# Performance work log

Hardware: AMD Instinct MI355X
Metric: run time of the kernel (lower is better)

The kernel has to match this reference:

```python
import jax, jax.numpy as jnp
import numpy as np

B, S, H, NH = 2, 2048, 2048, 16
HD = H // NH  # head_dim = 128


def setup_inputs() -> dict:
    key = jax.random.key(0)
    ks = jax.random.split(key, 6)
    scale = 1.0 / np.sqrt(H)
    hidden_state = jax.random.normal(ks[0], (B, S, H), dtype=jnp.float32)
    # upper-triangular (strictly above diagonal) = 1 -> masked positions
    causal_mask = jnp.triu(jnp.ones((S, S), dtype=jnp.float32), k=1)[None, None]
    Wq = jax.random.normal(ks[1], (H, H), dtype=jnp.float32) * scale
    Wk = jax.random.normal(ks[2], (H, H), dtype=jnp.float32) * scale
    Wv = jax.random.normal(ks[3], (H, H), dtype=jnp.float32) * scale
    Wo = jax.random.normal(ks[4], (H, H), dtype=jnp.float32) * scale
    zeros = jnp.zeros((H,), dtype=jnp.float32)
    return {"hidden_state": hidden_state, "causal_mask": causal_mask,
            "Wq": Wq, "bq": zeros, "Wk": Wk, "bk": zeros,
            "Wv": Wv, "bv": zeros, "Wo": Wo, "bo": zeros}


def reference(hidden_state, causal_mask, Wq, bq, Wk, bk, Wv, bv, Wo, bo):
    b, s, h = hidden_state.shape
    q = (hidden_state @ Wq.T + bq).reshape(b, s, NH, HD).transpose(0, 2, 1, 3)  # [B,NH,S,HD]
    k = (hidden_state @ Wk.T + bk).reshape(b, s, NH, HD).transpose(0, 2, 1, 3)
    v = (hidden_state @ Wv.T + bv).reshape(b, s, NH, HD).transpose(0, 2, 1, 3)
    scores = jnp.einsum('bhqd,bhkd->bhqk', q, k) / jnp.sqrt(jnp.float32(HD))
    scores = scores + causal_mask * (-1e9)
    probs = jax.nn.softmax(scores, axis=-1)
    out = jnp.einsum('bhqk,bhkd->bhqd', probs, v)
    out = out.transpose(0, 2, 1, 3).reshape(b, s, h)
    return out @ Wo.T + bo
```

## Files before the change

kernel.cpp:

```cpp
#include <hip/hip_runtime.h>
#include <hip/hip_bf16.h>
#include <stdint.h>

#define B_   2
#define S_   2048
#define H_   2048
#define NH_  16
#define HD_  128
#define MTOT (B_*S_)

typedef __attribute__((ext_vector_type(8))) short bf16x8;
typedef __attribute__((ext_vector_type(4))) short bf16x4;
typedef __attribute__((ext_vector_type(4))) float f32x4;

__device__ __forceinline__ void gload_lds16(const void* g, void* l) {
    __builtin_amdgcn_global_load_lds(
        (const __attribute__((address_space(1))) void*)g,
        (__attribute__((address_space(3))) void*)l, 16, 0, 0);
}

__device__ __forceinline__ unsigned short f2bfu(float x) {
    __hip_bfloat16 h = __float2bfloat16(x);
    return *reinterpret_cast<unsigned short*>(&h);
}
__device__ __forceinline__ int packbf(float a, float b) {
    return (int)f2bfu(a) | ((int)f2bfu(b) << 16);
}

#define BAR()  asm volatile("s_barrier" ::: "memory")
#define WLG0() asm volatile("s_waitcnt lgkmcnt(0)" ::: "memory")
#define WVM(n) asm volatile("s_waitcnt vmcnt(" #n ")" ::: "memory")

__global__ void castk(const float* __restrict__ in, __hip_bfloat16* __restrict__ out, int n4) {
    int i = blockIdx.x * 256 + threadIdx.x;
    if (i < n4) {
        float4 v = *(const float4*)(in + (size_t)i * 4);
        out[(size_t)i*4 + 0] = __float2bfloat16(v.x);
        out[(size_t)i*4 + 1] = __float2bfloat16(v.y);
        out[(size_t)i*4 + 2] = __float2bfloat16(v.z);
        out[(size_t)i*4 + 3] = __float2bfloat16(v.w);
    }
}

__global__ void castw4(const float* __restrict__ w0, const float* __restrict__ w1,
                       const float* __restrict__ w2, const float* __restrict__ w3,
                       __hip_bfloat16* o0, __hip_bfloat16* o1,
                       __hip_bfloat16* o2, __hip_bfloat16* o3, int n4) {
    const float* in; __hip_bfloat16* out;
    switch (blockIdx.y) {
        case 0:  in = w0; out = o0; break;
        case 1:  in = w1; out = o1; break;
        case 2:  in = w2; out = o2; break;
        default: in = w3; out = o3; break;
    }
    int i = blockIdx.x * 256 + threadIdx.x;
    if (i < n4) {
        float4 v = *(const float4*)(in + (size_t)i * 4);
        out[(size_t)i*4 + 0] = __float2bfloat16(v.x);
        out[(size_t)i*4 + 1] = __float2bfloat16(v.y);
        out[(size_t)i*4 + 2] = __float2bfloat16(v.z);
        out[(size_t)i*4 + 3] = __float2bfloat16(v.w);
    }
}

template<int SMEMB, int BF16OUT>
__device__ __forceinline__ void gemm_body(const __hip_bfloat16* __restrict__ Ablk,
                                          const __hip_bfloat16* __restrict__ Wblk,
                                          const float* __restrict__ bias,
                                          void* __restrict__ Cout,
                                          int N, int K, int br, int bc, bool vt)
{
    __shared__ __align__(16) char smem[SMEMB];
    __hip_bfloat16* As = (__hip_bfloat16*)smem;
    __hip_bfloat16* Bs = (__hip_bfloat16*)(smem + 8192);

    const int tid  = threadIdx.x;
    const int wave = tid >> 6, lane = tid & 63;
    const int quad = lane >> 4, l16 = lane & 15;
    const int wr = wave >> 1, wc = wave & 1;

    f32x4 acc[4][4] = {};

    for (int k0 = 0; k0 < K; k0 += 32) {
#pragma unroll
        for (int t = 0; t < 2; ++t) {
            int c = t * 256 + wave * 64 + lane;
            int row = c >> 2, cc = c & 3;
            int base = (t * 256 + wave * 64) * 16;
            gload_lds16(Ablk + (size_t)row * K + k0 + cc * 8, (char*)As + base);
            gload_lds16(Wblk + (size_t)row * K + k0 + cc * 8, (char*)Bs + base);
        }
        __syncthreads();

        bf16x8 af[4], bf[4];
#pragma unroll
        for (int i = 0; i < 4; ++i)
            af[i] = *(const bf16x8*)&As[(wr * 64 + i * 16 + l16) * 32 + quad * 8];
#pragma unroll
        for (int j = 0; j < 4; ++j)
            bf[j] = *(const bf16x8*)&Bs[(wc * 64 + j * 16 + l16) * 32 + quad * 8];

#pragma unroll
        for (int i = 0; i < 4; ++i)
#pragma unroll
            for (int j = 0; j < 4; ++j)
                acc[i][j] = __builtin_amdgcn_mfma_f32_16x16x32_bf16(af[i], bf[j], acc[i][j], 0, 0, 0);
        __syncthreads();
    }

    if (BF16OUT && vt) {
        __hip_bfloat16* Ls = (__hip_bfloat16*)smem;
#pragma unroll
        for (int j = 0; j < 4; ++j) {
            int d = wc * 64 + j * 16 + l16;
            float bv = bias[bc * 128 + d];
#pragma unroll
            for (int i = 0; i < 4; ++i) {
                int t0 = wr * 64 + i * 16 + quad * 4;
#pragma unroll
                for (int r = 0; r < 4; ++r)
                    Ls[d * 136 + t0 + r] = __float2bfloat16(acc[i][j][r] + bv);
            }
        }
        __syncthreads();
        const int bq = br >> 4;
        const int s0 = (br & 15) * 128;
        __hip_bfloat16* VT = (__hip_bfloat16*)Cout;
        const size_t rowbase = (size_t)(bq * 16 + bc) * 128;
#pragma unroll
        for (int rep = 0; rep < 8; ++rep) {
            int L = rep * 256 + tid;
            int d = L >> 4, tch = L & 15;
            bf16x8 v = *(const bf16x8*)&Ls[d * 136 + tch * 8];
            *(bf16x8*)(VT + (rowbase + d) * (size_t)S_ + s0 + tch * 8) = v;
        }
        return;
    }

#pragma unroll
    for (int i = 0; i < 4; ++i) {
        int row = br * 128 + wr * 64 + i * 16 + quad * 4;
#pragma unroll
        for (int j = 0; j < 4; ++j) {
            int col = bc * 128 + wc * 64 + j * 16 + l16;
            float bv = bias[col];
#pragma unroll
            for (int r = 0; r < 4; ++r) {
                float v = acc[i][j][r] + bv;
                if (BF16OUT)
                    ((__hip_bfloat16*)Cout)[(size_t)(row + r) * N + col] = __float2bfloat16(v);
                else
                    ((float*)Cout)[(size_t)(row + r) * N + col] = v;
            }
        }
    }
}

__global__ __launch_bounds__(256)
void gemm_out(const __hip_bfloat16* __restrict__ A, const __hip_bfloat16* __restrict__ W,
              const float* __restrict__ bias, float* __restrict__ C)
{
    gemm_body<16384, 0>(A + (size_t)(blockIdx.y * 128) * H_, W + (size_t)(blockIdx.x * 128) * H_,
                        bias, C, H_, H_, blockIdx.y, blockIdx.x, false);
}

__global__ __launch_bounds__(512, 2)
void gemm_qkv8(const __hip_bfloat16* __restrict__ X,
               const __hip_bfloat16* __restrict__ Wq, const __hip_bfloat16* __restrict__ Wk,
               const __hip_bfloat16* __restrict__ Wv,
               const float* __restrict__ bq, const float* __restrict__ bk,
               const float* __restrict__ bv,
               __hip_bfloat16* __restrict__ Qo, __hip_bfloat16* __restrict__ Ko,
               __hip_bfloat16* __restrict__ VTo)
{
    __shared__ __align__(16) char smem[131072];

    const int bid = blockIdx.x;
    const int swz = (bid & 7) * 48 + (bid >> 3);
    const int sel = swz >> 7;
    const int rem = swz & 127;
    const int bm  = rem & 15;
    const int bn  = rem >> 4;

    const __hip_bfloat16* W = (sel == 0) ? Wq : (sel == 1) ? Wk : Wv;
    const float* bias       = (sel == 0) ? bq : (sel == 1) ? bk : bv;

    const int tid  = threadIdx.x;
    const int wave = tid >> 6, lane = tid & 63;
    const int quad = lane >> 4, l16 = lane & 15;
    const int wr = wave >> 2, wc = wave & 3;

    const int ro = l16 * 64;
    const int co = (((l16 & 8) ? ((quad * 8) ^ 16) : (quad * 8)) << 1);

    int r0, c0, r1, c1;
    {
        int D = tid * 16;
        int rg = D >> 11, cg = (D >> 10) & 1;
        int rr = (D >> 6) & 15, c = (D & 63) >> 1;
        int cs = (rr & 8) ? (c ^ 16) : c;
        r0 = rg * 16 + rr;  c0 = cg * 32 + cs;
        D = 8192 + tid * 16;
        rg = D >> 11; cg = (D >> 10) & 1;
        rr = (D >> 6) & 15; c = (D & 63) >> 1;
        cs = (rr & 8) ? (c ^ 16) : c;
        r1 = rg * 16 + rr;  c1 = cg * 32 + cs;
    }

    const __hip_bfloat16* Xp = X + (size_t)(bm * 256) * H_;
    const __hip_bfloat16* Wp = W + (size_t)(bn * 256) * H_;

    char* const A0h = smem + wr * 16384;
    char* const A1h = smem + 32768 + wr * 16384;
    char* const B0h = smem + 65536 + (wc >> 1) * 16384;
    char* const B1h = smem + 98304 + (wc >> 1) * 16384;
    const int bsub = (wc & 1) * 4;

    auto STG = [&](char* ldsb, const __hip_bfloat16* g) {
        gload_lds16(g + (size_t)r0 * H_ + c0, ldsb + wave * 1024);
        gload_lds16(g + (size_t)r1 * H_ + c1, ldsb + 8192 + wave * 1024);
    };
    auto SRC = [&](const __hip_bfloat16* P, int t, int hf) {
        return P + (size_t)(hf * 128) * H_ + (size_t)t * 64;
    };

    f32x4 acc[8][4] = {};

    STG(smem,                 SRC(Xp, 0, 0));
    STG(smem + 16384,         SRC(Xp, 0, 1));
    STG(smem + 65536,         SRC(Wp, 0, 0));
    STG(smem + 65536 + 16384, SRC(Wp, 0, 1));
    STG(smem + 98304,         SRC(Wp, 1, 0));
    STG(smem + 98304 + 16384, SRC(Wp, 1, 1));
    WVM(4);
    BAR();

    const int NIT = H_ / 128;
    bf16x8 bfr[4][2];
    for (int j = 0; j < NIT; ++j) {
        const bool more = (j < NIT - 1);
        const int t1 = 2 * j + 1;
#pragma unroll
        for (int ph = 0; ph < 8; ++ph) {
            const int p = ph & 3;
            char* aA = (ph < 4) ? A0h : A1h;
            char* aB = (ph < 4) ? B0h : B1h;

            if (p == 0) {
#pragma unroll
                for (int jj = 0; jj < 4; ++jj)
#pragma unroll
                    for (int kk = 0; kk < 2; ++kk)
                        bfr[jj][kk] = *(const bf16x8*)(aB + ((bsub + jj) * 2 + kk) * 1024 + ro + co);
            }
            bf16x8 af[2][2];
#pragma unroll
            for (int i2 = 0; i2 < 2; ++i2)
#pragma unroll
                for (int kk = 0; kk < 2; ++kk)
                    af[i2][kk] = *(const bf16x8*)(aA + ((2 * p + i2) * 2 + kk) * 1024 + ro + co);

            if (ph == 0) { STG(smem + 32768, SRC(Xp, t1, 0));
                           STG(smem + 49152, SRC(Xp, t1, 1)); }
            else if (ph == 1 && more) STG(smem + 65536,          SRC(Wp, t1 + 1, 0));
            else if (ph == 2 && more) STG(smem + 65536 + 16384,  SRC(Wp, t1 + 1, 1));
            else if (ph == 4 && more) STG(smem,                  SRC(Xp, t1 + 1, 0));
            else if (ph == 5 && more) STG(smem + 16384,          SRC(Xp, t1 + 1, 1));
            else if (ph == 6 && more) STG(smem + 98304,          SRC(Wp, t1 + 2, 0));
            else if (ph == 7 && more) STG(smem + 98304 + 16384,  SRC(Wp, t1 + 2, 1));

            if (ph == 3) { if (more) { WVM(4); } else { WVM(0); } }
            if (ph == 7 && more) { WVM(4); }

            BAR();
            WLG0();
            __builtin_amdgcn_sched_barrier(0);
            __builtin_amdgcn_s_setprio(1);
#pragma unroll
            for (int kk = 0; kk < 2; ++kk)
#pragma unroll
                for (int i2 = 0; i2 < 2; ++i2)
#pragma unroll
                    for (int jj = 0; jj < 4; ++jj)
                        acc[2 * p + i2][jj] = __builtin_amdgcn_mfma_f32_16x16x32_bf16(
                            af[i2][kk], bfr[jj][kk], acc[2 * p + i2][jj], 0, 0, 0);
            __builtin_amdgcn_s_setprio(0);
            BAR();
        }
    }

    if (sel < 2) {
        __hip_bfloat16* out = (sel == 0) ? Qo : Ko;
#pragma unroll
        for (int i = 0; i < 8; ++i) {
            int row = bm * 256 + wr * 128 + i * 16 + quad * 4;
#pragma unroll
            for (int jj = 0; jj < 4; ++jj) {
                int col = bn * 256 + wc * 64 + jj * 16 + l16;
                float bv = bias[col];
#pragma unroll
                for (int r = 0; r < 4; ++r)
                    out[(size_t)(row + r) * H_ + col] = __float2bfloat16(acc[i][jj][r] + bv);
            }
        }
    } else {
#pragma unroll
        for (int i = 0; i < 8; ++i) {
            int tok = bm * 256 + wr * 128 + i * 16 + quad * 4;
            int b = tok >> 11, s = tok & (S_ - 1);
#pragma unroll
            for (int jj = 0; jj < 4; ++jj) {
                int col = bn * 256 + wc * 64 + jj * 16 + l16;
                int h = col >> 7, d = col & 127;
                float bv = bias[col];
                bf16x4 v;
#pragma unroll
                for (int r = 0; r < 4; ++r)
                    v[r] = (short)f2bfu(acc[i][jj][r] + bv);
                *(bf16x4*)(VTo + ((size_t)(b * 16 + h) * 128 + d) * S_ + s) = v;
            }
        }
    }
}

__global__ __launch_bounds__(256)
void attn_kernel(const __hip_bfloat16* __restrict__ Q,
                 const __hip_bfloat16* __restrict__ K,
                 const __hip_bfloat16* __restrict__ VT,
                 __hip_bfloat16* __restrict__ O)
{
    __shared__ __align__(16) char Ks[16384];
    __shared__ __align__(16) char Vt[16384];

    const int tid  = threadIdx.x;
    const int wave = tid >> 6, lane = tid & 63;
    const int quad = lane >> 4, l16 = lane & 15;

    const int lid = blockIdx.x;
    const int xcd = lid & 7;
    const int q   = lid >> 3;
    const int bh  = ((q >> 5) << 3) | xcd;
    const int qb  = 31 - (q & 31);
    const int b   = bh >> 4, h = bh & 15;

    const size_t headoff = (size_t)b * S_ * H_ + (size_t)h * HD_;
    const __hip_bfloat16* Qp  = Q + headoff;
    const __hip_bfloat16* Kp  = K + headoff;
    const __hip_bfloat16* Vtp = VT + (size_t)(b * 16 + h) * 128 * S_;

    const float scale = 0.08838834764831843f;
    const int A0 = (((quad & 1) * 2) * 16 + l16) * 4;
    const int A1 = A0 + 64;
    const bool hiq = (quad >= 2);

    const int qrow_local = wave * 16;
    const int qrow = qb * 64 + qrow_local;

    bf16x8 qf[4];
#pragma unroll
    for (int kd = 0; kd < 4; ++kd)
        qf[kd] = *(const bf16x8*)(Qp + (size_t)(qrow + l16) * H_ + kd * 32 + quad * 8);

    f32x4 oacc[8] = {};
    float mi = -1e30f, li = 0.0f;

#pragma unroll
    for (int t = 0; t < 4; ++t) {
        int c = wave * 256 + t * 64 + lane;
        int krow = c >> 4, kpos = c & 15;
        gload_lds16(Kp + (size_t)krow * H_ + (kpos ^ (krow & 7)) * 8,
                    &Ks[(wave * 256 + t * 64) * 16]);
        int vrow = c >> 3, vpos = c & 7;
        gload_lds16(Vtp + (size_t)vrow * S_ + (vpos ^ (vrow & 7)) * 8,
                    &Vt[(wave * 256 + t * 64) * 16]);
    }
    __syncthreads();

    for (int kb = 0; kb <= qb; ++kb) {
        const bool more = (kb < qb);

        f32x4 sacc[4] = {};
        __builtin_amdgcn_s_setprio(1);
#pragma unroll
        for (int cb = 0; cb < 4; ++cb) {
#pragma unroll
            for (int kd = 0; kd < 4; ++kd) {
                int row = cb * 16 + l16;
                int pos = (4 * kd + quad) ^ (l16 & 7);
                bf16x8 kf = *(const bf16x8*)&Ks[row * 256 + pos * 16];
                sacc[cb] = __builtin_amdgcn_mfma_f32_16x16x32_bf16(kf, qf[kd], sacc[cb], 0, 0, 0);
            }
        }
        __builtin_amdgcn_s_setprio(0);

        __syncthreads();

        if (more) {
            const __hip_bfloat16* Kn = Kp + (size_t)(kb + 1) * 64 * H_;
#pragma unroll
            for (int t = 0; t < 4; ++t) {
                int c = wave * 256 + t * 64 + lane;
                int krow = c >> 4, kpos = c & 15;
                gload_lds16(Kn + (size_t)krow * H_ + (kpos ^ (krow & 7)) * 8,
                            &Ks[(wave * 256 + t * 64) * 16]);
            }
        }

        const bool diag = (kb == qb);
        float p[4][4];
        float tm = -1e30f;
#pragma unroll
        for (int cb = 0; cb < 4; ++cb)
#pragma unroll
            for (int r = 0; r < 4; ++r) {
                float s = sacc[cb][r] * scale;
                if (diag) {
                    int keyl = cb * 16 + quad * 4 + r;
                    if (keyl > qrow_local + l16) s = -1e30f;
                }
                p[cb][r] = s;
                tm = fmaxf(tm, s);
            }
        tm = fmaxf(tm, __shfl_xor(tm, 16));
        tm = fmaxf(tm, __shfl_xor(tm, 32));
        float mnew = fmaxf(mi, tm);
        float sum = 0.0f;
#pragma unroll
        for (int cb = 0; cb < 4; ++cb)
#pragma unroll
            for (int r = 0; r < 4; ++r) {
                float e = __expf(p[cb][r] - mnew);
                p[cb][r] = e;
                sum += e;
            }
        sum += __shfl_xor(sum, 16);
        sum += __shfl_xor(sum, 32);
        float alpha = __expf(mi - mnew);
        li = li * alpha + sum;
        mi = mnew;

        float ar[4];
#pragma unroll
        for (int r = 0; r < 4; ++r)
            ar[r] = __shfl(alpha, quad * 4 + r);
#pragma unroll
        for (int db = 0; db < 8; ++db)
#pragma unroll
            for (int r = 0; r < 4; ++r)
                oacc[db][r] *= ar[r];

        int Pp[4][2];
#pragma unroll
        for (int cb = 0; cb < 4; ++cb) {
            Pp[cb][0] = packbf(p[cb][0], p[cb][1]);
            Pp[cb][1] = packbf(p[cb][2], p[cb][3]);
        }
        bf16x8 pf[2];
#pragma unroll
        for (int ks = 0; ks < 2; ++ks) {
            int c0 = 2 * ks, c1 = 2 * ks + 1;
            int d0 = __builtin_amdgcn_ds_bpermute(A0, Pp[c0][0]);
            int e0 = __builtin_amdgcn_ds_bpermute(A0, Pp[c1][0]);
            int d1 = __builtin_amdgcn_ds_bpermute(A0, Pp[c0][1]);
            int e1 = __builtin_amdgcn_ds_bpermute(A0, Pp[c1][1]);
            int d2 = __builtin_amdgcn_ds_bpermute(A1, Pp[c0][0]);
            int e2 = __builtin_amdgcn_ds_bpermute(A1, Pp[c1][0]);
            int d3 = __builtin_amdgcn_ds_bpermute(A1, Pp[c0][1]);
            int e3 = __builtin_amdgcn_ds_bpermute(A1, Pp[c1][1]);
            union { int i[4]; bf16x8 v; } u;
            u.i[0] = hiq ? e0 : d0;
            u.i[1] = hiq ? e1 : d1;
            u.i[2] = hiq ? e2 : d2;
            u.i[3] = hiq ? e3 : d3;
            pf[ks] = u.v;
        }

        __builtin_amdgcn_s_setprio(1);
#pragma unroll
        for (int ks = 0; ks < 2; ++ks) {
#pragma unroll
            for (int db = 0; db < 8; ++db) {
                int vrow = db * 16 + l16;
                int vpos = (ks * 4 + quad) ^ (l16 & 7);
                bf16x8 vf = *(const bf16x8*)&Vt[vrow * 128 + vpos * 16];
                oacc[db] = __builtin_amdgcn_mfma_f32_16x16x32_bf16(pf[ks], vf, oacc[db], 0, 0, 0);
            }
        }
        __builtin_amdgcn_s_setprio(0);

        __syncthreads();

        if (more) {
            const int vcol = (kb + 1) * 64;
#pragma unroll
            for (int t = 0; t < 4; ++t) {
                int c = wave * 256 + t * 64 + lane;
                int vrow = c >> 3, vpos = c & 7;
                gload_lds16(Vtp + (size_t)vrow * S_ + vcol + (vpos ^ (vrow & 7)) * 8,
                            &Vt[(wave * 256 + t * 64) * 16]);
            }
        }
    }

    float lr[4];
#pragma unroll
    for (int r = 0; r < 4; ++r)
        lr[r] = __shfl(li, quad * 4 + r);
#pragma unroll
    for (int db = 0; db < 8; ++db)
#pragma unroll
        for (int r = 0; r < 4; ++r) {
            float v = oacc[db][r] / lr[r];
            size_t row = (size_t)b * S_ + qrow + quad * 4 + r;
            O[row * H_ + h * HD_ + db * 16 + l16] = __float2bfloat16(v);
        }
}

extern "C" void kernel_launch(void* const* d_in, const int* in_sizes, int n_in,
                              void* d_out, int out_size, void* d_ws, size_t ws_size,
                              hipStream_t stream)
{
    const float* hs = (const float*)d_in[0];
    const float* Wq = (const float*)d_in[2];
    const float* bq = (const float*)d_in[3];
    const float* Wk = (const float*)d_in[4];
    const float* bk = (const float*)d_in[5];
    const float* Wv = (const float*)d_in[6];
    const float* bv = (const float*)d_in[7];
    const float* Wo = (const float*)d_in[8];
    const float* bo = (const float*)d_in[9];

    const size_t szX = (size_t)MTOT * H_;
    const size_t szW = (size_t)H_ * H_;

    __hip_bfloat16* Xbf = (__hip_bfloat16*)d_ws;
    __hip_bfloat16* Wqb = Xbf + szX;
    __hip_bfloat16* Wkb = Wqb + szW;
    __hip_bfloat16* Wvb = Wkb + szW;
    __hip_bfloat16* Wob = Wvb + szW;
    __hip_bfloat16* Qb  = Wob + szW;
    __hip_bfloat16* Kb  = Qb + szX;
    __hip_bfloat16* VTb = Kb + szX;

    castk<<<(int)((szX/4 + 255)/256), 256, 0, stream>>>(hs, Xbf, (int)(szX/4));
    dim3 wgrid((unsigned)((szW/4 + 255)/256), 4);
    castw4<<<wgrid, 256, 0, stream>>>(Wq, Wk, Wv, Wo, Wqb, Wkb, Wvb, Wob, (int)(szW/4));

    gemm_qkv8<<<dim3(384), 512, 0, stream>>>(Xbf, Wqb, Wkb, Wvb, bq, bk, bv, Qb, Kb, VTb);

    attn_kernel<<<dim3(1024), 256, 0, stream>>>(Qb, Kb, VTb, Xbf);

    gemm_out<<<dim3(16, 32), 256, 0, stream>>>(Xbf, Wob, bo, (float*)d_out);
}
```

Baseline: 421.8 us.

## Merge cast kernels, template QKV epilogue, and skip softmax rescale when max grows little

The two fp32-to-bf16 cast kernels become one launch over a 6-row grid covering the hidden state and all four weights. The QKV GEMM body is split into a templated helper so the V-transpose and the plain row-major epilogues are chosen at compile time, and the unused V-transpose path in the small GEMM is deleted. In attention, the online softmax keeps the old running max and skips the rescale of the output accumulator whenever every lane's new tile max exceeds it by at most 8, which saves shuffles and multiplies at the risk of larger exponent values. The s_setprio hints around the MFMA loops are removed.

```diff
diff --git a/kernel.cpp b/kernel.cpp
--- a/kernel.cpp
+++ b/kernel.cpp
@@ -31,36 +31,29 @@
 #define WLG0() asm volatile("s_waitcnt lgkmcnt(0)" ::: "memory")
 #define WVM(n) asm volatile("s_waitcnt vmcnt(" #n ")" ::: "memory")
 
-__global__ void castk(const float* __restrict__ in, __hip_bfloat16* __restrict__ out, int n4) {
-    int i = blockIdx.x * 256 + threadIdx.x;
-    if (i < n4) {
-        float4 v = *(const float4*)(in + (size_t)i * 4);
-        out[(size_t)i*4 + 0] = __float2bfloat16(v.x);
-        out[(size_t)i*4 + 1] = __float2bfloat16(v.y);
-        out[(size_t)i*4 + 2] = __float2bfloat16(v.z);
-        out[(size_t)i*4 + 3] = __float2bfloat16(v.w);
-    }
-}
-
-__global__ void castw4(const float* __restrict__ w0, const float* __restrict__ w1,
-                       const float* __restrict__ w2, const float* __restrict__ w3,
-                       __hip_bfloat16* o0, __hip_bfloat16* o1,
-                       __hip_bfloat16* o2, __hip_bfloat16* o3, int n4) {
-    const float* in; __hip_bfloat16* out;
+__global__ void castall(const float* __restrict__ hs,
+                        const float* __restrict__ w0, const float* __restrict__ w1,
+                        const float* __restrict__ w2, const float* __restrict__ w3,
+                        __hip_bfloat16* __restrict__ xb,
+                        __hip_bfloat16* __restrict__ o0, __hip_bfloat16* __restrict__ o1,
+                        __hip_bfloat16* __restrict__ o2, __hip_bfloat16* __restrict__ o3)
+{
+    const size_t Q = 1048576;
+    const float* in; __hip_bfloat16* out; size_t base;
     switch (blockIdx.y) {
-        case 0:  in = w0; out = o0; break;
-        case 1:  in = w1; out = o1; break;
-        case 2:  in = w2; out = o2; break;
-        default: in = w3; out = o3; break;
-    }
-    int i = blockIdx.x * 256 + threadIdx.x;
-    if (i < n4) {
-        float4 v = *(const float4*)(in + (size_t)i * 4);
-        out[(size_t)i*4 + 0] = __float2bfloat16(v.x);
-        out[(size_t)i*4 + 1] = __float2bfloat16(v.y);
-        out[(size_t)i*4 + 2] = __float2bfloat16(v.z);
-        out[(size_t)i*4 + 3] = __float2bfloat16(v.w);
-    }
+        case 0:  in = hs; out = xb; base = 0; break;
+        case 1:  in = hs; out = xb; base = Q; break;
+        case 2:  in = w0; out = o0; base = 0; break;
+        case 3:  in = w1; out = o1; base = 0; break;
+        case 4:  in = w2; out = o2; base = 0; break;
+        default: in = w3; out = o3; base = 0; break;
+    }
+    size_t i = base + (size_t)blockIdx.x * 256 + threadIdx.x;
+    float4 v = *(const float4*)(in + i * 4);
+    out[i*4 + 0] = __float2bfloat16(v.x);
+    out[i*4 + 1] = __float2bfloat16(v.y);
+    out[i*4 + 2] = __float2bfloat16(v.z);
+    out[i*4 + 3] = __float2bfloat16(v.w);
 }
 
 template<int SMEMB, int BF16OUT>
@@ -68,7 +61,7 @@
                                           const __hip_bfloat16* __restrict__ Wblk,
                                           const float* __restrict__ bias,
                                           void* __restrict__ Cout,
-                                          int N, int K, int br, int bc, bool vt)
+                                          int N, int K, int br, int bc)
 {
     __shared__ __align__(16) char smem[SMEMB];
     __hip_bfloat16* As = (__hip_bfloat16*)smem;
@@ -108,35 +101,6 @@
         __syncthreads();
     }
 
-    if (BF16OUT && vt) {
-        __hip_bfloat16* Ls = (__hip_bfloat16*)smem;
-#pragma unroll
-        for (int j = 0; j < 4; ++j) {
-            int d = wc * 64 + j * 16 + l16;
-            float bv = bias[bc * 128 + d];
-#pragma unroll
-            for (int i = 0; i < 4; ++i) {
-                int t0 = wr * 64 + i * 16 + quad * 4;
-#pragma unroll
-                for (int r = 0; r < 4; ++r)
-                    Ls[d * 136 + t0 + r] = __float2bfloat16(acc[i][j][r] + bv);
-            }
-        }
-        __syncthreads();
-        const int bq = br >> 4;
-        const int s0 = (br & 15) * 128;
-        __hip_bfloat16* VT = (__hip_bfloat16*)Cout;
-        const size_t rowbase = (size_t)(bq * 16 + bc) * 128;
-#pragma unroll
-        for (int rep = 0; rep < 8; ++rep) {
-            int L = rep * 256 + tid;
-            int d = L >> 4, tch = L & 15;
-            bf16x8 v = *(const bf16x8*)&Ls[d * 136 + tch * 8];
-            *(bf16x8*)(VT + (rowbase + d) * (size_t)S_ + s0 + tch * 8) = v;
-        }
-        return;
-    }
-
 #pragma unroll
     for (int i = 0; i < 4; ++i) {
         int row = br * 128 + wr * 64 + i * 16 + quad * 4;
@@ -161,30 +125,16 @@
               const float* __restrict__ bias, float* __restrict__ C)
 {
     gemm_body<16384, 0>(A + (size_t)(blockIdx.y * 128) * H_, W + (size_t)(blockIdx.x * 128) * H_,
-                        bias, C, H_, H_, blockIdx.y, blockIdx.x, false);
-}
-
-__global__ __launch_bounds__(512, 2)
-void gemm_qkv8(const __hip_bfloat16* __restrict__ X,
-               const __hip_bfloat16* __restrict__ Wq, const __hip_bfloat16* __restrict__ Wk,
-               const __hip_bfloat16* __restrict__ Wv,
-               const float* __restrict__ bq, const float* __restrict__ bk,
-               const float* __restrict__ bv,
-               __hip_bfloat16* __restrict__ Qo, __hip_bfloat16* __restrict__ Ko,
-               __hip_bfloat16* __restrict__ VTo)
-{
-    __shared__ __align__(16) char smem[131072];
-
-    const int bid = blockIdx.x;
-    const int swz = (bid & 7) * 48 + (bid >> 3);
-    const int sel = swz >> 7;
-    const int rem = swz & 127;
-    const int bm  = rem & 15;
-    const int bn  = rem >> 4;
-
-    const __hip_bfloat16* W = (sel == 0) ? Wq : (sel == 1) ? Wk : Wv;
-    const float* bias       = (sel == 0) ? bq : (sel == 1) ? bk : bv;
-
+                        bias, C, H_, H_, blockIdx.y, blockIdx.x);
+}
+
+template<int EPI>
+__device__ __forceinline__ void gemm256_body(const __hip_bfloat16* __restrict__ Xp,
+                                             const __hip_bfloat16* __restrict__ Wp,
+                                             const float* __restrict__ bias,
+                                             void* __restrict__ Cout,
+                                             int bm, int bn, char* smem)
+{
     const int tid  = threadIdx.x;
     const int wave = tid >> 6, lane = tid & 63;
     const int quad = lane >> 4, l16 = lane & 15;
@@ -207,9 +157,6 @@
         r1 = rg * 16 + rr;  c1 = cg * 32 + cs;
     }
 
-    const __hip_bfloat16* Xp = X + (size_t)(bm * 256) * H_;
-    const __hip_bfloat16* Wp = W + (size_t)(bn * 256) * H_;
-
     char* const A0h = smem + wr * 16384;
     char* const A1h = smem + 32768 + wr * 16384;
     char* const B0h = smem + 65536 + (wc >> 1) * 16384;
@@ -289,21 +236,8 @@
         }
     }
 
-    if (sel < 2) {
-        __hip_bfloat16* out = (sel == 0) ? Qo : Ko;
-#pragma unroll
-        for (int i = 0; i < 8; ++i) {
-            int row = bm * 256 + wr * 128 + i * 16 + quad * 4;
-#pragma unroll
-            for (int jj = 0; jj < 4; ++jj) {
-                int col = bn * 256 + wc * 64 + jj * 16 + l16;
-                float bv = bias[col];
-#pragma unroll
-                for (int r = 0; r < 4; ++r)
-                    out[(size_t)(row + r) * H_ + col] = __float2bfloat16(acc[i][jj][r] + bv);
-            }
-        }
-    } else {
+    if (EPI == 2) {
+        __hip_bfloat16* VTo = (__hip_bfloat16*)Cout;
 #pragma unroll
         for (int i = 0; i < 8; ++i) {
             int tok = bm * 256 + wr * 128 + i * 16 + quad * 4;
@@ -320,7 +254,51 @@
                 *(bf16x4*)(VTo + ((size_t)(b * 16 + h) * 128 + d) * S_ + s) = v;
             }
         }
-    }
+    } else {
+#pragma unroll
+        for (int i = 0; i < 8; ++i) {
+            int row = bm * 256 + wr * 128 + i * 16 + quad * 4;
+#pragma unroll
+            for (int jj = 0; jj < 4; ++jj) {
+                int col = bn * 256 + wc * 64 + jj * 16 + l16;
+                float bv = bias[col];
+#pragma unroll
+                for (int r = 0; r < 4; ++r)
+                    ((__hip_bfloat16*)Cout)[(size_t)(row + r) * H_ + col] =
+                        __float2bfloat16(acc[i][jj][r] + bv);
+            }
+        }
+    }
+}
+
+__global__ __launch_bounds__(512, 2)
+void gemm_qkv8(const __hip_bfloat16* __restrict__ X,
+               const __hip_bfloat16* __restrict__ Wq, const __hip_bfloat16* __restrict__ Wk,
+               const __hip_bfloat16* __restrict__ Wv,
+               const float* __restrict__ bq, const float* __restrict__ bk,
+               const float* __restrict__ bv,
+               __hip_bfloat16* __restrict__ Qo, __hip_bfloat16* __restrict__ Ko,
+               __hip_bfloat16* __restrict__ VTo)
+{
+    __shared__ __align__(16) char smem[131072];
+
+    const int bid = blockIdx.x;
+    const int swz = (bid & 7) * 48 + (bid >> 3);
+    const int sel = swz >> 7;
+    const int rem = swz & 127;
+    const int bm  = rem & 15;
+    const int bn  = rem >> 4;
+
+    const __hip_bfloat16* W = (sel == 0) ? Wq : (sel == 1) ? Wk : Wv;
+    const float* bias       = (sel == 0) ? bq : (sel == 1) ? bk : bv;
+
+    const __hip_bfloat16* Xp = X + (size_t)(bm * 256) * H_;
+    const __hip_bfloat16* Wp = W + (size_t)(bn * 256) * H_;
+
+    if (sel == 2)
+        gemm256_body<2>(Xp, Wp, bias, VTo, bm, bn, smem);
+    else
+        gemm256_body<1>(Xp, Wp, bias, (sel == 0) ? Qo : Ko, bm, bn, smem);
 }
 
 __global__ __launch_bounds__(256)
@@ -380,7 +358,6 @@
         const bool more = (kb < qb);
 
         f32x4 sacc[4] = {};
-        __builtin_amdgcn_s_setprio(1);
 #pragma unroll
         for (int cb = 0; cb < 4; ++cb) {
 #pragma unroll
@@ -391,7 +368,6 @@
                 sacc[cb] = __builtin_amdgcn_mfma_f32_16x16x32_bf16(kf, qf[kd], sacc[cb], 0, 0, 0);
             }
         }
-        __builtin_amdgcn_s_setprio(0);
 
         __syncthreads();
 
@@ -423,7 +399,10 @@
             }
         tm = fmaxf(tm, __shfl_xor(tm, 16));
         tm = fmaxf(tm, __shfl_xor(tm, 32));
-        float mnew = fmaxf(mi, tm);
+
+        const bool noresc = __all(tm - mi <= 8.0f);
+        float mnew = noresc ? mi : fmaxf(mi, tm);
+
         float sum = 0.0f;
 #pragma unroll
         for (int cb = 0; cb < 4; ++cb)
@@ -435,19 +414,23 @@
             }
         sum += __shfl_xor(sum, 16);
         sum += __shfl_xor(sum, 32);
-        float alpha = __expf(mi - mnew);
-        li = li * alpha + sum;
+
+        if (noresc) {
+            li = li + sum;
+        } else {
+            float alpha = __expf(mi - mnew);
+            li = li * alpha + sum;
+            float ar[4];
+#pragma unroll
+            for (int r = 0; r < 4; ++r)
+                ar[r] = __shfl(alpha, quad * 4 + r);
+#pragma unroll
+            for (int db = 0; db < 8; ++db)
+#pragma unroll
+                for (int r = 0; r < 4; ++r)
+                    oacc[db][r] *= ar[r];
+        }
         mi = mnew;
-
-        float ar[4];
-#pragma unroll
-        for (int r = 0; r < 4; ++r)
-            ar[r] = __shfl(alpha, quad * 4 + r);
-#pragma unroll
-        for (int db = 0; db < 8; ++db)
-#pragma unroll
-            for (int r = 0; r < 4; ++r)
-                oacc[db][r] *= ar[r];
 
         int Pp[4][2];
 #pragma unroll
@@ -475,7 +458,6 @@
             pf[ks] = u.v;
         }
 
-        __builtin_amdgcn_s_setprio(1);
 #pragma unroll
         for (int ks = 0; ks < 2; ++ks) {
 #pragma unroll
@@ -486,7 +468,6 @@
                 oacc[db] = __builtin_amdgcn_mfma_f32_16x16x32_bf16(pf[ks], vf, oacc[db], 0, 0, 0);
             }
         }
-        __builtin_amdgcn_s_setprio(0);
 
         __syncthreads();
 
@@ -542,9 +523,7 @@
     __hip_bfloat16* Kb  = Qb + szX;
     __hip_bfloat16* VTb = Kb + szX;
 
-    castk<<<(int)((szX/4 + 255)/256), 256, 0, stream>>>(hs, Xbf, (int)(szX/4));
-    dim3 wgrid((unsigned)((szW/4 + 255)/256), 4);
-    castw4<<<wgrid, 256, 0, stream>>>(Wq, Wk, Wv, Wo, Wqb, Wkb, Wvb, Wob, (int)(szW/4));
+    castall<<<dim3(4096, 6), 256, 0, stream>>>(hs, Wq, Wk, Wv, Wo, Xbf, Wqb, Wkb, Wvb, Wob);
 
     gemm_qkv8<<<dim3(384), 512, 0, stream>>>(Xbf, Wqb, Wkb, Wvb, bq, bk, bv, Qb, Kb, VTb);
 
```

Result: faster. 406.9 us (-3.5%).
